# Kernel tuning notes

Hardware: AMD Instinct MI355X
Metric: run time of the kernel (lower is better)

## Reference

```python
import jax, jax.numpy as jnp
import numpy as np

NEG_SLOPE = 0.2  # PyG GATConv default


def gat_layer(x, src, dst, W, a_src, a_dst, b, heads, ch, num_nodes):
    # x: [N, F_in]; W: [F_in, heads*ch]; a_src/a_dst: [heads, ch]; b: [heads*ch]
    h = (x @ W).reshape(num_nodes, heads, ch)                      # [N,H,C]
    al_s = jnp.einsum('nhc,hc->nh', h, a_src)                      # [N,H]
    al_d = jnp.einsum('nhc,hc->nh', h, a_dst)                      # [N,H]
    e = jax.nn.leaky_relu(al_s[src] + al_d[dst], NEG_SLOPE)        # [E,H]
    # segment softmax over incoming edges of each destination node
    emax = jax.ops.segment_max(e, dst, num_segments=num_nodes)     # [N,H]
    ee = jnp.exp(e - emax[dst])
    denom = jax.ops.segment_sum(ee, dst, num_segments=num_nodes)   # [N,H]
    alpha = ee / denom[dst]                                        # [E,H]
    msg = h[src] * alpha[..., None]                                # [E,H,C]
    out = jax.ops.segment_sum(msg, dst, num_segments=num_nodes)    # [N,H,C]
    return out.reshape(num_nodes, heads * ch) + b


def setup_inputs() -> dict:
    key = jax.random.key(0)
    ks = jax.random.split(key, 12)
    N, F_in, H1, C1, OUT = 50000, 128, 6, 32, 2
    E = 800000
    x = jax.random.normal(ks[0], (N, F_in), dtype=jnp.float32)
    edge_index = jax.random.randint(ks[1], (2, E), 0, N, dtype=jnp.int64)
    s = 0.1
    return {
        'x': x,
        'edge_index': edge_index,
        'W1': jax.random.normal(ks[2], (F_in, H1 * C1), dtype=jnp.float32) * s,
        'a1_src': jax.random.normal(ks[3], (H1, C1), dtype=jnp.float32) * s,
        'a1_dst': jax.random.normal(ks[4], (H1, C1), dtype=jnp.float32) * s,
        'b1': jnp.zeros((H1 * C1,), dtype=jnp.float32),
        'W2': jax.random.normal(ks[5], (H1 * C1, 1 * OUT), dtype=jnp.float32) * s,
        'a2_src': jax.random.normal(ks[6], (1, OUT), dtype=jnp.float32) * s,
        'a2_dst': jax.random.normal(ks[7], (1, OUT), dtype=jnp.float32) * s,
        'b2': jnp.zeros((OUT,), dtype=jnp.float32),
    }


def reference(x, edge_index, W1, a1_src, a1_dst, b1, W2, a2_src, a2_dst, b2):
    N = x.shape[0]
    loop = jnp.arange(N, dtype=edge_index.dtype)
    src = jnp.concatenate([edge_index[0], loop])  # add_self_loops=True (PyG default)
    dst = jnp.concatenate([edge_index[1], loop])
    h = gat_layer(x, src, dst, W1, a1_src, a1_dst, b1, heads=6, ch=32, num_nodes=N)
    h = jax.nn.relu(h)
    h = gat_layer(h, src, dst, W2, a2_src, a2_dst, b2, heads=1, ch=2, num_nodes=N)
    return jax.nn.log_softmax(h, axis=1)
```

## Files before the change

kernel.cpp:

```cpp
#include <hip/hip_runtime.h>
#include <hip/hip_fp16.h>

#define LRELU(v) ((v) > 0.0f ? (v) : 0.2f * (v))

constexpr int F_IN = 128;
constexpr int NH1  = 6;
constexpr int D1   = 192;

typedef _Float16 half8 __attribute__((ext_vector_type(8)));
typedef _Float16 half4v __attribute__((ext_vector_type(4)));
typedef float floatx4 __attribute__((ext_vector_type(4)));

__device__ __forceinline__ void wave_lds_fence() {
  __builtin_amdgcn_wave_barrier();
  asm volatile("s_waitcnt lgkmcnt(0)" ::: "memory");
  __builtin_amdgcn_wave_barrier();
}

__global__ __launch_bounds__(256) void k_hist(const float* __restrict__ W1,
                                              __half* __restrict__ w1t,
                                              const int* __restrict__ dst,
                                              int* __restrict__ cnt,
                                              int* __restrict__ pose, int E) {
  int tid = blockIdx.x * 256 + threadIdx.x;
  if (tid < F_IN * D1) {
    int k = tid / D1, n = tid - k * D1;
    w1t[(size_t)n * F_IN + k] = __float2half(W1[tid]);
  }
  if (tid < E) {
    pose[tid] = atomicAdd(&cnt[dst[tid]], 1);
  }
}

__global__ void k_scanA(const int* __restrict__ cnt, int* __restrict__ offs,
                        int* __restrict__ bsum, int N) {
  int base = cnt[N];
  int t = threadIdx.x;
  int idx = blockIdx.x * 256 + t;
  int lane = t & 63, w = t >> 6;
  int v = (idx < N) ? (cnt[idx] - base) : 0;
  int incl = v;
#pragma unroll
  for (int d = 1; d < 64; d <<= 1) {
    int u = __shfl_up(incl, d);
    if (lane >= d) incl += u;
  }
  __shared__ int wt[4];
  if (lane == 63) wt[w] = incl;
  __syncthreads();
  int woff = 0;
  for (int i = 0; i < w; ++i) woff += wt[i];
  if (idx < N) offs[idx] = woff + incl - v;
  if (t == 255) bsum[blockIdx.x] = woff + incl;
}

__global__ __launch_bounds__(256) void k_scanC2(int* __restrict__ offs,
                                                const int* __restrict__ bsum,
                                                int N, int NB) {
  __shared__ int sh[2];
  int t = threadIdx.x;
  if (t < 64) {
    int pre = 0, tot = 0;
#pragma unroll
    for (int r = 0; r < 4; ++r) {
      int i = r * 64 + t;
      int b = (i < NB) ? bsum[i] : 0;
      if (i < (int)blockIdx.x) pre += b;
      tot += b;
    }
#pragma unroll
    for (int m = 32; m; m >>= 1) {
      pre += __shfl_xor(pre, m);
      tot += __shfl_xor(tot, m);
    }
    if (t == 0) { sh[0] = pre; sh[1] = tot; }
  }
  __syncthreads();
  int idx = blockIdx.x * 256 + t;
  if (idx < N) offs[idx] += sh[0];
  if (idx == 0) offs[N] = sh[1];
}

__global__ __launch_bounds__(256) void k_gp(
    const float* __restrict__ x, const __half* __restrict__ w1t,
    const float* __restrict__ a1s, const float* __restrict__ a1d,
    __half* __restrict__ h1h, float* __restrict__ als, float* __restrict__ ald,
    const int* __restrict__ src, const int* __restrict__ dst,
    const int* __restrict__ offs, const int* __restrict__ pose,
    const int* __restrict__ cnt,
    int* __restrict__ ssort, int N, int E, int GB) {
  if ((int)blockIdx.x >= GB) {
    int base = cnt[N];
    int e = ((int)blockIdx.x - GB) * 256 + threadIdx.x;
    if (e < E) ssort[offs[dst[e]] + (pose[e] - base)] = src[e];
    return;
  }

  int wv = blockIdx.x * 4 + (threadIdx.x >> 6);
  int m0 = wv * 16;
  if (m0 >= N) return;
  int lane = threadIdx.x & 63;
  int ln15 = lane & 15, q = lane >> 4;

  float avs[12], avd[12];
#pragma unroll
  for (int f = 0; f < 12; ++f) {
    int idx = (f >> 1) * 32 + (f & 1) * 16 + ln15;
    avs[f] = a1s[idx];
    avd[f] = a1d[idx];
  }

  floatx4 acc[12];
#pragma unroll
  for (int f = 0; f < 12; ++f) acc[f] = (floatx4){0.f, 0.f, 0.f, 0.f};

  int arowi = m0 + ln15;
  if (arowi >= N) arowi = N - 1;
  const float* arow = x + (size_t)arowi * F_IN + q * 8;
#pragma unroll
  for (int kc = 0; kc < F_IN; kc += 32) {
    float4 u0 = *(const float4*)(arow + kc);
    float4 u1 = *(const float4*)(arow + kc + 4);
    half8 a;
    a[0] = (_Float16)u0.x; a[1] = (_Float16)u0.y; a[2] = (_Float16)u0.z; a[3] = (_Float16)u0.w;
    a[4] = (_Float16)u1.x; a[5] = (_Float16)u1.y; a[6] = (_Float16)u1.z; a[7] = (_Float16)u1.w;
#pragma unroll
    for (int f = 0; f < 12; ++f) {
      half8 b = *(const half8*)(w1t + (size_t)(16 * f + ln15) * F_IN + kc + q * 8);
      acc[f] = __builtin_amdgcn_mfma_f32_16x16x32_f16(a, b, acc[f], 0, 0, 0);
    }
  }

#pragma unroll
  for (int f = 0; f < 12; ++f) {
#pragma unroll
    for (int r = 0; r < 4; ++r) {
      int n = m0 + q * 4 + r;
      if (n < N) h1h[(size_t)n * D1 + 16 * f + ln15] = __float2half(acc[f][r]);
    }
  }

#pragma unroll
  for (int r = 0; r < 4; ++r) {
    float ps[6] = {0.f, 0.f, 0.f, 0.f, 0.f, 0.f};
    float pd[6] = {0.f, 0.f, 0.f, 0.f, 0.f, 0.f};
#pragma unroll
    for (int f = 0; f < 12; ++f) {
      ps[f >> 1] = fmaf(acc[f][r], avs[f], ps[f >> 1]);
      pd[f >> 1] = fmaf(acc[f][r], avd[f], pd[f >> 1]);
    }
#pragma unroll
    for (int h = 0; h < 6; ++h) {
#pragma unroll
      for (int m = 8; m; m >>= 1) {
        ps[h] += __shfl_xor(ps[h], m);
        pd[h] += __shfl_xor(pd[h], m);
      }
    }
    float os = 0.f, od = 0.f;
#pragma unroll
    for (int h = 0; h < 6; ++h)
      if (ln15 == h) { os = ps[h]; od = pd[h]; }
    int n = m0 + q * 4 + r;
    if (ln15 < 6 && n < N) {
      als[(size_t)n * 6 + ln15] = os;
      ald[(size_t)n * 6 + ln15] = od;
    }
  }
}

__global__ __launch_bounds__(256) void k_agg1(
    const __half* __restrict__ h1h, const float* __restrict__ als, const float* __restrict__ ald,
    const int* __restrict__ offs, const int* __restrict__ srcs,
    const float* __restrict__ b1, const float* __restrict__ W2,
    const float* __restrict__ a2s, const float* __restrict__ a2d,
    float4* __restrict__ pk, int N) {
  __shared__ float wbuf[4][64][9];
  int wid = threadIdx.x >> 6, lane = threadIdx.x & 63;
  int d = blockIdx.x * 4 + wid;
  if (d >= N) return;
  int off = offs[d], cnt = offs[d + 1] - off;
  int tot = cnt + 1;

  float aldh[6];
  {
    const float* ap = ald + (size_t)d * 6;
    float2 q0 = *(const float2*)ap, q1 = *(const float2*)(ap + 2), q2 = *(const float2*)(ap + 4);
    aldh[0] = q0.x; aldh[1] = q0.y; aldh[2] = q1.x;
    aldh[3] = q1.y; aldh[4] = q2.x; aldh[5] = q2.y;
  }

  float dh[6] = {0.f, 0.f, 0.f, 0.f, 0.f, 0.f};
  int nchunk = (tot + 63) >> 6;

  const bool act = lane < 48;
  const int hd = lane >> 3;
  float a0 = 0.f, a1 = 0.f, a2 = 0.f, a3 = 0.f;

  auto body = [&](int j) {
    float w = wbuf[wid][j][hd < 6 ? hd : 0];
    int soff = __float_as_int(wbuf[wid][j][6]);
    const __half* hp = (const __half*)((const char*)h1h + soff);
    half4v v = *(const half4v*)(hp + 4 * lane);
    a0 = fmaf(w, (float)v[0], a0);
    a1 = fmaf(w, (float)v[1], a1);
    a2 = fmaf(w, (float)v[2], a2);
    a3 = fmaf(w, (float)v[3], a3);
  };
  auto jloop = [&](int jmax) {
    int j = 0;
    for (; j + 3 < jmax; j += 4) { body(j); body(j + 1); body(j + 2); body(j + 3); }
    for (; j < jmax; ++j) body(j);
  };

  if (nchunk == 1) {
    float wreg[6];
    int sreg = 0;
    if (lane < tot) {
      int s = (lane == cnt) ? d : srcs[off + lane];
      sreg = s;
      const float* ap = als + (size_t)s * 6;
      float2 p0 = *(const float2*)ap, p1 = *(const float2*)(ap + 2), p2 = *(const float2*)(ap + 4);
      float ev[6] = {p0.x, p0.y, p1.x, p1.y, p2.x, p2.y};
#pragma unroll
      for (int h = 0; h < 6; ++h) {
        float e = ev[h] + aldh[h];
        e = LRELU(e);
        wreg[h] = __expf(e);
        dh[h] = wreg[h];
      }
    }
#pragma unroll
    for (int h = 0; h < 6; ++h) {
#pragma unroll
      for (int m = 32; m; m >>= 1) dh[h] += __shfl_xor(dh[h], m);
      dh[h] = 1.0f / dh[h];
    }
    if (lane < tot) {
#pragma unroll
      for (int h = 0; h < 6; ++h) wbuf[wid][lane][h] = wreg[h] * dh[h];
      wbuf[wid][lane][6] = __int_as_float(sreg * (D1 * 2));
    }
    wave_lds_fence();
    if (act) jloop(tot);
  } else {
    for (int c = 0; c < nchunk; ++c) {
      int i = c * 64 + lane;
      if (i < tot) {
        int s = (i == cnt) ? d : srcs[off + i];
        const float* ap = als + (size_t)s * 6;
        float2 p0 = *(const float2*)ap, p1 = *(const float2*)(ap + 2), p2 = *(const float2*)(ap + 4);
        float ev[6] = {p0.x, p0.y, p1.x, p1.y, p2.x, p2.y};
#pragma unroll
        for (int h = 0; h < 6; ++h) {
          float e = ev[h] + aldh[h];
          e = LRELU(e);
          dh[h] += __expf(e);
        }
      }
    }
#pragma unroll
    for (int h = 0; h < 6; ++h) {
#pragma unroll
      for (int m = 32; m; m >>= 1) dh[h] += __shfl_xor(dh[h], m);
      dh[h] = 1.0f / dh[h];
    }
    for (int c = 0; c < nchunk; ++c) {
      int i = c * 64 + lane;
      if (i < tot) {
        int s = (i == cnt) ? d : srcs[off + i];
        const float* ap = als + (size_t)s * 6;
        float2 p0 = *(const float2*)ap, p1 = *(const float2*)(ap + 2), p2 = *(const float2*)(ap + 4);
        float ev[6] = {p0.x, p0.y, p1.x, p1.y, p2.x, p2.y};
#pragma unroll
        for (int h = 0; h < 6; ++h) {
          float e = ev[h] + aldh[h];
          e = LRELU(e);
          wbuf[wid][lane][h] = __expf(e) * dh[h];
        }
        wbuf[wid][lane][6] = __int_as_float(s * (D1 * 2));
      }
      wave_lds_fence();
      int jmax = tot - c * 64;
      if (jmax > 64) jmax = 64;
      if (act) jloop(jmax);
      wave_lds_fence();
    }
  }

  float s0 = 0.f, s1 = 0.f;
  if (act) {
    float4 bv = *(const float4*)(b1 + 4 * lane);
    float v0 = fmaxf(a0 + bv.x, 0.f);
    float v1 = fmaxf(a1 + bv.y, 0.f);
    float v2 = fmaxf(a2 + bv.z, 0.f);
    float v3 = fmaxf(a3 + bv.w, 0.f);
    float4 w01 = *(const float4*)(W2 + 8 * lane);
    float4 w23 = *(const float4*)(W2 + 8 * lane + 4);
    s0 = v0 * w01.x + v1 * w01.z + v2 * w23.x + v3 * w23.z;
    s1 = v0 * w01.y + v1 * w01.w + v2 * w23.y + v3 * w23.w;
  }
#pragma unroll
  for (int m = 32; m; m >>= 1) {
    s0 += __shfl_xor(s0, m);
    s1 += __shfl_xor(s1, m);
  }
  if (lane == 0) {
    pk[d] = make_float4(s0, s1,
                        s0 * a2s[0] + s1 * a2s[1],
                        s0 * a2d[0] + s1 * a2d[1]);
  }
}

__global__ __launch_bounds__(256) void k_agg2(
    const float4* __restrict__ pk, const int* __restrict__ offs,
    const int* __restrict__ srcs, const float* __restrict__ b2,
    float* __restrict__ out, int N) {
  int tid = blockIdx.x * 256 + threadIdx.x;
  int g = tid >> 3, r = tid & 7;
  if (g >= N) return;
  int off = offs[g], cnt = offs[g + 1] - off;
  int tot = cnt + 1;
  float ad = pk[g].w;
  float den = 0.f, o0 = 0.f, o1 = 0.f;
  for (int i = r; i < tot; i += 8) {
    int s = (i == cnt) ? g : srcs[off + i];
    float4 p = pk[s];
    float e = p.z + ad;
    e = LRELU(e);
    float a = __expf(e);
    den += a;
    o0 = fmaf(a, p.x, o0);
    o1 = fmaf(a, p.y, o1);
  }
#pragma unroll
  for (int m = 4; m; m >>= 1) {
    den += __shfl_xor(den, m);
    o0 += __shfl_xor(o0, m);
    o1 += __shfl_xor(o1, m);
  }
  if (r == 0) {
    float inv = 1.0f / den;
    o0 = o0 * inv + b2[0];
    o1 = o1 * inv + b2[1];
    float mm = fmaxf(o0, o1);
    float l = mm + logf(__expf(o0 - mm) + __expf(o1 - mm));
    *(float2*)(out + (size_t)g * 2) = make_float2(o0 - l, o1 - l);
  }
}

extern "C" void kernel_launch(void* const* d_in, const int* in_sizes, int n_in,
                              void* d_out, int out_size, void* d_ws, size_t ws_size,
                              hipStream_t stream) {
  const float* x   = (const float*)d_in[0];
  const int*   ei  = (const int*)d_in[1];
  const float* W1  = (const float*)d_in[2];
  const float* a1s = (const float*)d_in[3];
  const float* a1d = (const float*)d_in[4];
  const float* b1  = (const float*)d_in[5];
  const float* W2  = (const float*)d_in[6];
  const float* a2s = (const float*)d_in[7];
  const float* a2d = (const float*)d_in[8];
  const float* b2  = (const float*)d_in[9];
  float* out = (float*)d_out;

  const int N = in_sizes[0] / F_IN;
  const int E = in_sizes[1] / 2;
  const int* srcp = ei;
  const int* dstp = ei + E;

  char* w = (char*)d_ws;
  auto alloc = [&](size_t bytes) {
    char* p = w;
    w += (bytes + 255) & ~(size_t)255;
    return p;
  };
  __half* h1h   = (__half*)alloc((size_t)N * D1 * 2 + 256);
  __half* w1t   = (__half*)alloc((size_t)F_IN * D1 * 2);
  float* als    = (float*)alloc((size_t)N * NH1 * 4);
  float* ald    = (float*)alloc((size_t)N * NH1 * 4);
  float4* pk    = (float4*)alloc((size_t)N * 16);
  int*   cnt    = (int*)alloc((size_t)(N + 1) * 4);
  int*   offs   = (int*)alloc((size_t)(N + 1) * 4);
  int*   pose   = (int*)alloc((size_t)E * 4);
  int*   ssort  = (int*)alloc((size_t)E * 4);
  int*   bsum   = (int*)alloc(1024);

  const int NB = (N + 255) / 256;
  const int GB = ((N + 15) / 16 + 3) / 4;
  const int PB = (E + 255) / 256;

  k_hist<<<(E + 255) / 256, 256, 0, stream>>>(W1, w1t, dstp, cnt, pose, E);
  k_scanA<<<NB, 256, 0, stream>>>(cnt, offs, bsum, N);
  k_scanC2<<<NB, 256, 0, stream>>>(offs, bsum, N, NB);
  k_gp<<<GB + PB, 256, 0, stream>>>(x, w1t, a1s, a1d, h1h, als, ald,
                                    srcp, dstp, offs, pose, cnt, ssort, N, E, GB);
  k_agg1<<<(N + 3) / 4, 256, 0, stream>>>(h1h, als, ald, offs, ssort, b1, W2,
                                          a2s, a2d, pk, N);
  k_agg2<<<(N * 8 + 255) / 256, 256, 0, stream>>>(pk, offs, ssort, b2, out, N);
}
```

Measured before the change: 224.0 us.

## Fold block-offset scan into consumers and use half2 FMA in aggregation

Removes the k_scanC2 launch. Each consumer kernel (scatter, agg1, agg2) now rebuilds the block-prefix table from bsum in shared memory and adds it to the local offsets. Separately, agg1 stores the attention weights as half2 and accumulates features with packed half2 FMAs instead of fp32 FMAs. This saves one launch and halves the ALU work in the gather loop. The costs are redundant per-block scan work in every consumer block and reduced accumulation precision, since fp16 sums may hurt accuracy for high-degree nodes.

```diff
diff --git a/kernel.cpp b/kernel.cpp
--- a/kernel.cpp
+++ b/kernel.cpp
@@ -8,13 +8,35 @@
 constexpr int D1   = 192;
 
 typedef _Float16 half8 __attribute__((ext_vector_type(8)));
-typedef _Float16 half4v __attribute__((ext_vector_type(4)));
 typedef float floatx4 __attribute__((ext_vector_type(4)));
 
 __device__ __forceinline__ void wave_lds_fence() {
   __builtin_amdgcn_wave_barrier();
   asm volatile("s_waitcnt lgkmcnt(0)" ::: "memory");
   __builtin_amdgcn_wave_barrier();
+}
+
+__device__ __forceinline__ void build_btab(const int* __restrict__ bsum, int NB,
+                                           int* btab, int* btot) {
+  if (threadIdx.x < 64) {
+    int lane = threadIdx.x;
+    int carry = 0;
+#pragma unroll
+    for (int r = 0; r < 4; ++r) {
+      int i = r * 64 + lane;
+      int v = (i < NB) ? bsum[i] : 0;
+      int incl = v;
+#pragma unroll
+      for (int d = 1; d < 64; d <<= 1) {
+        int u = __shfl_up(incl, d);
+        if (lane >= d) incl += u;
+      }
+      btab[i] = carry + incl - v;
+      carry += __shfl(incl, 63);
+    }
+    if (lane == 0) *btot = carry;
+  }
+  __syncthreads();
 }
 
 __global__ __launch_bounds__(256) void k_hist(const float* __restrict__ W1,
@@ -54,45 +76,24 @@
   if (t == 255) bsum[blockIdx.x] = woff + incl;
 }
 
-__global__ __launch_bounds__(256) void k_scanC2(int* __restrict__ offs,
-                                                const int* __restrict__ bsum,
-                                                int N, int NB) {
-  __shared__ int sh[2];
-  int t = threadIdx.x;
-  if (t < 64) {
-    int pre = 0, tot = 0;
-#pragma unroll
-    for (int r = 0; r < 4; ++r) {
-      int i = r * 64 + t;
-      int b = (i < NB) ? bsum[i] : 0;
-      if (i < (int)blockIdx.x) pre += b;
-      tot += b;
-    }
-#pragma unroll
-    for (int m = 32; m; m >>= 1) {
-      pre += __shfl_xor(pre, m);
-      tot += __shfl_xor(tot, m);
-    }
-    if (t == 0) { sh[0] = pre; sh[1] = tot; }
-  }
-  __syncthreads();
-  int idx = blockIdx.x * 256 + t;
-  if (idx < N) offs[idx] += sh[0];
-  if (idx == 0) offs[N] = sh[1];
-}
-
 __global__ __launch_bounds__(256) void k_gp(
     const float* __restrict__ x, const __half* __restrict__ w1t,
     const float* __restrict__ a1s, const float* __restrict__ a1d,
     __half* __restrict__ h1h, float* __restrict__ als, float* __restrict__ ald,
     const int* __restrict__ src, const int* __restrict__ dst,
     const int* __restrict__ offs, const int* __restrict__ pose,
-    const int* __restrict__ cnt,
-    int* __restrict__ ssort, int N, int E, int GB) {
+    const int* __restrict__ cnt, const int* __restrict__ bsum,
+    int* __restrict__ ssort, int N, int E, int GB, int NB) {
   if ((int)blockIdx.x >= GB) {
+    __shared__ int btab[256];
+    __shared__ int btot;
+    build_btab(bsum, NB, btab, &btot);
     int base = cnt[N];
     int e = ((int)blockIdx.x - GB) * 256 + threadIdx.x;
-    if (e < E) ssort[offs[dst[e]] + (pose[e] - base)] = src[e];
+    if (e < E) {
+      int d = dst[e];
+      ssort[offs[d] + btab[d >> 8] + (pose[e] - base)] = src[e];
+    }
     return;
   }
 
@@ -172,14 +173,21 @@
 __global__ __launch_bounds__(256) void k_agg1(
     const __half* __restrict__ h1h, const float* __restrict__ als, const float* __restrict__ ald,
     const int* __restrict__ offs, const int* __restrict__ srcs,
+    const int* __restrict__ bsum,
     const float* __restrict__ b1, const float* __restrict__ W2,
     const float* __restrict__ a2s, const float* __restrict__ a2d,
-    float4* __restrict__ pk, int N) {
+    float4* __restrict__ pk, int N, int NB) {
+  __shared__ int btab[256];
+  __shared__ int btot;
   __shared__ float wbuf[4][64][9];
+  build_btab(bsum, NB, btab, &btot);
+
   int wid = threadIdx.x >> 6, lane = threadIdx.x & 63;
   int d = blockIdx.x * 4 + wid;
   if (d >= N) return;
-  int off = offs[d], cnt = offs[d + 1] - off;
+  int off = offs[d] + btab[d >> 8];
+  int end = (d + 1 < N) ? (offs[d + 1] + btab[(d + 1) >> 8]) : btot;
+  int cnt = end - off;
   int tot = cnt + 1;
 
   float aldh[6];
@@ -195,17 +203,14 @@
 
   const bool act = lane < 48;
   const int hd = lane >> 3;
-  float a0 = 0.f, a1 = 0.f, a2 = 0.f, a3 = 0.f;
+  __half2 a01 = __float2half2_rn(0.f), a23 = __float2half2_rn(0.f);
 
   auto body = [&](int j) {
-    float w = wbuf[wid][j][hd < 6 ? hd : 0];
+    __half2 w = *(__half2*)&wbuf[wid][j][hd < 6 ? hd : 0];
     int soff = __float_as_int(wbuf[wid][j][6]);
-    const __half* hp = (const __half*)((const char*)h1h + soff);
-    half4v v = *(const half4v*)(hp + 4 * lane);
-    a0 = fmaf(w, (float)v[0], a0);
-    a1 = fmaf(w, (float)v[1], a1);
-    a2 = fmaf(w, (float)v[2], a2);
-    a3 = fmaf(w, (float)v[3], a3);
+    const __half2* hp = (const __half2*)((const char*)h1h + soff + 8 * lane);
+    a01 = __hfma2(w, hp[0], a01);
+    a23 = __hfma2(w, hp[1], a23);
   };
   auto jloop = [&](int jmax) {
     int j = 0;
@@ -238,7 +243,8 @@
     }
     if (lane < tot) {
 #pragma unroll
-      for (int h = 0; h < 6; ++h) wbuf[wid][lane][h] = wreg[h] * dh[h];
+      for (int h = 0; h < 6; ++h)
+        *(__half2*)&wbuf[wid][lane][h] = __float2half2_rn(wreg[h] * dh[h]);
       wbuf[wid][lane][6] = __int_as_float(sreg * (D1 * 2));
     }
     wave_lds_fence();
@@ -276,7 +282,7 @@
         for (int h = 0; h < 6; ++h) {
           float e = ev[h] + aldh[h];
           e = LRELU(e);
-          wbuf[wid][lane][h] = __expf(e) * dh[h];
+          *(__half2*)&wbuf[wid][lane][h] = __float2half2_rn(__expf(e) * dh[h]);
         }
         wbuf[wid][lane][6] = __int_as_float(s * (D1 * 2));
       }
@@ -290,11 +296,13 @@
 
   float s0 = 0.f, s1 = 0.f;
   if (act) {
+    float2 f01 = __half22float2(a01);
+    float2 f23 = __half22float2(a23);
     float4 bv = *(const float4*)(b1 + 4 * lane);
-    float v0 = fmaxf(a0 + bv.x, 0.f);
-    float v1 = fmaxf(a1 + bv.y, 0.f);
-    float v2 = fmaxf(a2 + bv.z, 0.f);
-    float v3 = fmaxf(a3 + bv.w, 0.f);
+    float v0 = fmaxf(f01.x + bv.x, 0.f);
+    float v1 = fmaxf(f01.y + bv.y, 0.f);
+    float v2 = fmaxf(f23.x + bv.z, 0.f);
+    float v3 = fmaxf(f23.y + bv.w, 0.f);
     float4 w01 = *(const float4*)(W2 + 8 * lane);
     float4 w23 = *(const float4*)(W2 + 8 * lane + 4);
     s0 = v0 * w01.x + v1 * w01.z + v2 * w23.x + v3 * w23.z;
@@ -314,12 +322,19 @@
 
 __global__ __launch_bounds__(256) void k_agg2(
     const float4* __restrict__ pk, const int* __restrict__ offs,
-    const int* __restrict__ srcs, const float* __restrict__ b2,
-    float* __restrict__ out, int N) {
+    const int* __restrict__ srcs, const int* __restrict__ bsum,
+    const float* __restrict__ b2,
+    float* __restrict__ out, int N, int NB) {
+  __shared__ int btab[256];
+  __shared__ int btot;
+  build_btab(bsum, NB, btab, &btot);
+
   int tid = blockIdx.x * 256 + threadIdx.x;
   int g = tid >> 3, r = tid & 7;
   if (g >= N) return;
-  int off = offs[g], cnt = offs[g + 1] - off;
+  int off = offs[g] + btab[g >> 8];
+  int end = (g + 1 < N) ? (offs[g + 1] + btab[(g + 1) >> 8]) : btot;
+  int cnt = end - off;
   int tot = cnt + 1;
   float ad = pk[g].w;
   float den = 0.f, o0 = 0.f, o1 = 0.f;
@@ -392,10 +407,10 @@
 
   k_hist<<<(E + 255) / 256, 256, 0, stream>>>(W1, w1t, dstp, cnt, pose, E);
   k_scanA<<<NB, 256, 0, stream>>>(cnt, offs, bsum, N);
-  k_scanC2<<<NB, 256, 0, stream>>>(offs, bsum, N, NB);
   k_gp<<<GB + PB, 256, 0, stream>>>(x, w1t, a1s, a1d, h1h, als, ald,
-                                    srcp, dstp, offs, pose, cnt, ssort, N, E, GB);
-  k_agg1<<<(N + 3) / 4, 256, 0, stream>>>(h1h, als, ald, offs, ssort, b1, W2,
-                                          a2s, a2d, pk, N);
-  k_agg2<<<(N * 8 + 255) / 256, 256, 0, stream>>>(pk, offs, ssort, b2, out, N);
-}
+                                    srcp, dstp, offs, pose, cnt, bsum,
+                                    ssort, N, E, GB, NB);
+  k_agg1<<<(N + 3) / 4, 256, 0, stream>>>(h1h, als, ald, offs, ssort, bsum,
+                                          b1, W2, a2s, a2d, pk, N, NB);
+  k_agg2<<<(N * 8 + 255) / 256, 256, 0, stream>>>(pk, offs, ssort, bsum, b2, out, N, NB);
+}
```

Measured after the change: 235.8 us. 1.05x slower.
